# Optimization experiments

Measured on AMD Instinct MI355X. Metric: run time of the kernel, lower is better.

The kernel has to match this reference:

```python
import jax, jax.numpy as jnp
import numpy as np

D_MODEL, D_STATE, D_CONV, EXPAND = 512, 16, 2, 2
D_INNER = EXPAND * D_MODEL          # 1024
DT_RANK = (D_MODEL + 15) // 16      # 32, mamba default ceil(d_model/16)
D_FF = 4 * D_MODEL                  # 2048
B, L = 8, 2048


def _mamba_params(key, prefix):
    ks = jax.random.split(key, 6)
    s = lambda k, shape, sc: (jax.random.normal(k, shape, jnp.float32) * sc)
    return {
        prefix + 'in_proj': s(ks[0], (2 * D_INNER, D_MODEL), 0.02),
        prefix + 'conv_w':  s(ks[1], (D_INNER, 1, D_CONV), 0.2),
        prefix + 'conv_b':  jnp.zeros((D_INNER,), jnp.float32),
        prefix + 'x_proj':  s(ks[2], (DT_RANK + 2 * D_STATE, D_INNER), 0.02),
        prefix + 'dt_w':    s(ks[3], (D_INNER, DT_RANK), 0.05),
        prefix + 'dt_b':    s(ks[4], (D_INNER,), 0.02) - 4.0,  # softplus -> small positive dt
        prefix + 'A_log':   jnp.log(jnp.broadcast_to(jnp.arange(1, D_STATE + 1, dtype=jnp.float32), (D_INNER, D_STATE))),
        prefix + 'Dskip':   jnp.ones((D_INNER,), jnp.float32),
        prefix + 'out_proj': s(ks[5], (D_MODEL, D_INNER), 0.02),
    }


def setup_inputs() -> dict:
    key = jax.random.key(0)
    kx, kf, kb, k1, k2, k3, k4 = jax.random.split(key, 7)
    inp = {'x': jax.random.normal(kx, (B, L, D_MODEL), jnp.float32)}
    inp.update(_mamba_params(kf, 'f_'))
    inp.update(_mamba_params(kb, 'b_'))
    inp.update({
        'ffn_w1': jax.random.normal(k1, (D_FF, D_MODEL), jnp.float32) * 0.02,
        'ffn_b1': jnp.zeros((D_FF,), jnp.float32),
        'ffn_w2': jax.random.normal(k2, (D_MODEL, D_FF), jnp.float32) * 0.02,
        'ffn_b2': jnp.zeros((D_MODEL,), jnp.float32),
        'ln1_g': jnp.ones((D_MODEL,), jnp.float32), 'ln1_b': jnp.zeros((D_MODEL,), jnp.float32),
        'ln2_g': jnp.ones((D_MODEL,), jnp.float32), 'ln2_b': jnp.zeros((D_MODEL,), jnp.float32),
    })
    return inp


def _mamba(x, in_proj, conv_w, conv_b, x_proj, dt_w, dt_b, A_log, Dskip, out_proj):
    """Standard Mamba block (selective SSM). x: (B, L, d_model) -> (B, L, d_model)."""
    Bb = x.shape[0]
    xz = jnp.einsum('bld,ed->ble', x, in_proj)         # (B, L, 2*d_inner)
    xi, z = jnp.split(xz, 2, axis=-1)
    # causal depthwise conv over time
    xc = jnp.transpose(xi, (0, 2, 1))                  # (B, d_inner, L)
    xc = jax.lax.conv_general_dilated(
        xc, conv_w, (1,), [(D_CONV - 1, 0)],
        dimension_numbers=('NCH', 'OIH', 'NCH'), feature_group_count=D_INNER)
    xi = jax.nn.silu(jnp.transpose(xc, (0, 2, 1)) + conv_b)  # (B, L, d_inner)
    # input-dependent dt, B, C
    x_dbl = jnp.einsum('bld,ed->ble', xi, x_proj)
    dt, Bm, Cm = jnp.split(x_dbl, [DT_RANK, DT_RANK + D_STATE], axis=-1)
    dt = jax.nn.softplus(jnp.einsum('blr,dr->bld', dt, dt_w) + dt_b)  # (B, L, d_inner)
    A = -jnp.exp(A_log)                                 # (d_inner, d_state)

    def step(h, inp):
        u_t, dt_t, B_t, C_t = inp                      # (B,d_inner),(B,d_inner),(B,d_state),(B,d_state)
        dA = jnp.exp(dt_t[..., None] * A)              # (B, d_inner, d_state)
        h = dA * h + (dt_t * u_t)[..., None] * B_t[:, None, :]
        y = jnp.einsum('bds,bs->bd', h, C_t)
        return h, y

    h0 = jnp.zeros((Bb, D_INNER, D_STATE), x.dtype)
    xs = (jnp.swapaxes(xi, 0, 1), jnp.swapaxes(dt, 0, 1),
          jnp.swapaxes(Bm, 0, 1), jnp.swapaxes(Cm, 0, 1))
    _, ys = jax.lax.scan(step, h0, xs)                 # ys: (L, B, d_inner)
    y = jnp.swapaxes(ys, 0, 1) + xi * Dskip
    y = y * jax.nn.silu(z)
    return jnp.einsum('bld,ed->ble', y, out_proj)


def _ln(x, g, b):
    m = x.mean(-1, keepdims=True)
    v = ((x - m) ** 2).mean(-1, keepdims=True)
    return (x - m) * jax.lax.rsqrt(v + 1e-5) * g + b


def reference(x,
              f_in_proj, f_conv_w, f_conv_b, f_x_proj, f_dt_w, f_dt_b, f_A_log, f_Dskip, f_out_proj,
              b_in_proj, b_conv_w, b_conv_b, b_x_proj, b_dt_w, b_dt_b, b_A_log, b_Dskip, b_out_proj,
              ffn_w1, ffn_b1, ffn_w2, ffn_b2, ln1_g, ln1_b, ln2_g, ln2_b):
    x_fwd = _mamba(x, f_in_proj, f_conv_w, f_conv_b, f_x_proj, f_dt_w, f_dt_b, f_A_log, f_Dskip, f_out_proj)
    x_bwd = jnp.flip(_mamba(jnp.flip(x, 1), b_in_proj, b_conv_w, b_conv_b, b_x_proj, b_dt_w, b_dt_b, b_A_log, b_Dskip, b_out_proj), 1)
    x = _ln(x + x_fwd + x_bwd, ln1_g, ln1_b)           # dropout = identity (eval)
    h = jax.nn.gelu(jnp.einsum('bld,fd->blf', x, ffn_w1) + ffn_b1, approximate=False)
    x_ffn = jnp.einsum('blf,df->bld', h, ffn_w2) + ffn_b2
    return _ln(x + x_ffn, ln2_g, ln2_b)
```

## Files before the change

### kernel.cpp

```cpp
#include <hip/hip_runtime.h>
#include <hip/hip_bf16.h>

#define BB 8
#define LL 2048
#define DM 512
#define DI 1024
#define DS 16
#define DTR 32
#define DFF 2048
#define BL (BB * LL)
#define CH 64
#define NCH (LL / CH)
#define YL 2048

typedef __hip_bfloat16 bf16;
struct bf4 { bf16 x, y, z, w; };
typedef __attribute__((ext_vector_type(8))) short short8;
typedef __attribute__((ext_vector_type(4))) float floatx4;

__device__ __forceinline__ float silu_f(float x) { return x / (1.f + __expf(-x)); }
__device__ __forceinline__ float softplus_f(float x) { return x > 20.f ? x : log1pf(__expf(x)); }
__device__ __forceinline__ float gelu_f(float x) { return 0.5f * x * (1.f + erff(x * 0.70710678118654752f)); }
__device__ __forceinline__ float b2f(bf16 v) { return __bfloat162float(v); }

__device__ __forceinline__ float4 ld4(const float* p) { return *(const float4*)p; }
__device__ __forceinline__ float4 ld4(const bf16* p) {
    bf4 v = *(const bf4*)p;
    return make_float4(b2f(v.x), b2f(v.y), b2f(v.z), b2f(v.w));
}
__device__ __forceinline__ bf4 pack4(float a, float b, float c, float d) {
    bf4 o; o.x = __float2bfloat16(a); o.y = __float2bfloat16(b);
    o.z = __float2bfloat16(c); o.w = __float2bfloat16(d); return o;
}

__device__ __forceinline__ void gll16(const bf16* g, bf16* l) {
    __builtin_amdgcn_global_load_lds(
        (const __attribute__((address_space(1))) void*)g,
        (__attribute__((address_space(3))) void*)l, 16, 0, 0);
}

enum { EP_BF16, EP_SOFTPLUS, EP_GELU, EP_F32, EP_RESF, EP_BIASRES };

__global__ __launch_bounds__(256) void cvt_kernel(const float* __restrict__ in,
                                                  bf16* __restrict__ out, int n4)
{
    int i = blockIdx.x * 256 + threadIdx.x;
    if (i < n4) {
        float4 v = *(const float4*)(in + (size_t)i * 4);
        *(bf4*)(out + (size_t)i * 4) = pack4(v.x, v.y, v.z, v.w);
    }
}

__global__ __launch_bounds__(256) void cvt_pack_kernel(
    const float* __restrict__ wf, const float* __restrict__ wb,
    bf16* __restrict__ out, int n4)
{
    int i = blockIdx.x * 256 + threadIdx.x;
    if (i < n4) {
        const int pos = i * 4;
        const int n = pos >> 11;
        const int c = pos & 2047;
        const float* src = (c < 1024) ? (wf + (size_t)n * 1024 + c)
                                      : (wb + (size_t)n * 1024 + (c - 1024));
        float4 v = *(const float4*)src;
        *(bf4*)(out + (size_t)pos) = pack4(v.x, v.y, v.z, v.w);
    }
}

template <int EPI, int BN>
__global__ __launch_bounds__(256) void gemm_mfma(
    const bf16* __restrict__ A, int lda,
    const bf16* __restrict__ W, int ldb,
    void* __restrict__ Cv, int ldc, int K,
    const float* __restrict__ bias, const void* __restrict__ resv)
{
    constexpr int BM = 128, BK = 32;
    constexpr int NT = BN / 32;
    constexpr int ACH_W = 2;
    constexpr int WCH_W = (BN / 16) / 4;
    constexpr int PITCH = BN + 8;
    constexpr int TILE_B = BM * 64 + BN * 64;
    constexpr int STG_B = 32 * PITCH * 4;
    constexpr int SMEM_B = TILE_B > STG_B ? TILE_B : STG_B;
    __shared__ __align__(1024) char smem[SMEM_B];
    bf16* sA = (bf16*)smem;
    bf16* sW = (bf16*)(smem + BM * 64);

    const int tid = threadIdx.x;
    const int wv = tid >> 6, ln = tid & 63;
    const int rloc = ln >> 2;
    const int kperm = (ln & 3) ^ ((ln >> 3) & 3);
    const int c = ln & 15, q4 = ln >> 4;
    const int swz8 = 8 * (q4 ^ ((c >> 1) & 3));
    const int m0 = blockIdx.x * BM, n0 = blockIdx.y * BN;
    const int wm = (wv >> 1) * 64, wn = (wv & 1) * (BN / 2);

    floatx4 acc[4][NT] = {};

    for (int k0 = 0; k0 < K; k0 += BK) {
        __syncthreads();
#pragma unroll
        for (int q = 0; q < ACH_W; ++q) {
            const int chunk = wv * ACH_W + q;
            gll16(A + (size_t)(m0 + chunk * 16 + rloc) * lda + k0 + kperm * 8,
                  sA + chunk * 512);
        }
#pragma unroll
        for (int q = 0; q < WCH_W; ++q) {
            const int chunk = wv * WCH_W + q;
            gll16(W + (size_t)(n0 + chunk * 16 + rloc) * ldb + k0 + kperm * 8,
                  sW + chunk * 512);
        }
        __syncthreads();

        short8 af[4], wf[NT];
#pragma unroll
        for (int i = 0; i < 4; ++i)
            af[i] = *(const short8*)(sA + (wm + i * 16 + c) * 32 + swz8);
#pragma unroll
        for (int j = 0; j < NT; ++j)
            wf[j] = *(const short8*)(sW + (wn + j * 16 + c) * 32 + swz8);
#pragma unroll
        for (int i = 0; i < 4; ++i)
#pragma unroll
            for (int j = 0; j < NT; ++j)
                acc[i][j] = __builtin_amdgcn_mfma_f32_16x16x32_bf16(
                    af[i], wf[j], acc[i][j], 0, 0, 0);
    }

    constexpr int ELEMS = (32 * BN) / 256;
    constexpr int TPR = BN / ELEMS;
    float* sC = (float*)smem;
    const int row_l = tid / TPR;
    const int cg = (tid % TPR) * ELEMS;
    const int mg = m0 + (row_l & 15) + ((row_l >> 4) * 64);

#pragma unroll
    for (int i = 0; i < 4; ++i) {
        __syncthreads();
#pragma unroll
        for (int j = 0; j < NT; ++j)
#pragma unroll
            for (int r = 0; r < 4; ++r)
                sC[((wv >> 1) * 16 + q4 * 4 + r) * PITCH + wn + j * 16 + c] = acc[i][j][r];
        __syncthreads();

        const int m = mg + i * 16;
        const int nb = n0 + cg;
        const size_t co = (size_t)m * ldc + nb;
        float v[ELEMS];
#pragma unroll
        for (int e = 0; e < ELEMS; ++e) v[e] = sC[row_l * PITCH + cg + e];

        if constexpr (EPI == EP_BF16 || EPI == EP_GELU) {
            bf16 ov[ELEMS];
#pragma unroll
            for (int e = 0; e < ELEMS; ++e) {
                float t = v[e];
                if constexpr (EPI == EP_GELU) t = gelu_f(t + bias[nb + e]);
                ov[e] = __float2bfloat16(t);
            }
#pragma unroll
            for (int q = 0; q < ELEMS / 8; ++q)
                *(uint4*)((bf16*)Cv + co + q * 8) = *(const uint4*)(ov + q * 8);
        } else {
#pragma unroll
            for (int e = 0; e < ELEMS; ++e) {
                if constexpr (EPI == EP_RESF)
                    v[e] += ((const float*)resv)[co + e];
                else if constexpr (EPI == EP_BIASRES)
                    v[e] += bias[nb + e] + b2f(((const bf16*)resv)[co + e]);
            }
#pragma unroll
            for (int q = 0; q < ELEMS / 4; ++q) {
                float4 o = {v[q * 4 + 0], v[q * 4 + 1], v[q * 4 + 2], v[q * 4 + 3]};
                *(float4*)((float*)Cv + co + q * 4) = o;
            }
        }
    }
}

template <int EPI, typename TA>
__global__ __launch_bounds__(256) void gemm_nt(
    const TA* __restrict__ A, int lda,
    const float* __restrict__ W, int ldb,
    void* __restrict__ Cv, int ldc,
    int K,
    const float* __restrict__ bias,
    const void* __restrict__ resv)
{
    __shared__ float As[16][64];
    __shared__ float Bs[16][64];
    const int tid = threadIdx.x;
    const int tx = tid & 15, ty = tid >> 4;
    const int m0 = blockIdx.y * 64, n0 = blockIdx.x * 64;
    const int lrow = tid >> 2;
    const int lcol = (tid & 3) << 2;

    const TA* Ap = A + (size_t)(m0 + lrow) * lda + lcol;
    const float* Bp = W + (size_t)(n0 + lrow) * ldb + lcol;

    float acc[4][4] = {};

    for (int k0 = 0; k0 < K; k0 += 16) {
        float4 av = ld4(Ap + k0);
        float4 bv = ld4(Bp + k0);
        __syncthreads();
        As[lcol + 0][lrow] = av.x; As[lcol + 1][lrow] = av.y;
        As[lcol + 2][lrow] = av.z; As[lcol + 3][lrow] = av.w;
        Bs[lcol + 0][lrow] = bv.x; Bs[lcol + 1][lrow] = bv.y;
        Bs[lcol + 2][lrow] = bv.z; Bs[lcol + 3][lrow] = bv.w;
        __syncthreads();
#pragma unroll
        for (int kk = 0; kk < 16; ++kk) {
            float4 a4 = *(const float4*)(&As[kk][ty << 2]);
            float4 b4 = *(const float4*)(&Bs[kk][tx << 2]);
            float aa[4] = {a4.x, a4.y, a4.z, a4.w};
            float bb[4] = {b4.x, b4.y, b4.z, b4.w};
#pragma unroll
            for (int i = 0; i < 4; ++i)
#pragma unroll
                for (int j = 0; j < 4; ++j)
                    acc[i][j] = fmaf(aa[i], bb[j], acc[i][j]);
        }
    }

#pragma unroll
    for (int i = 0; i < 4; ++i) {
        const int m = m0 + (ty << 2) + i;
        const int n = n0 + (tx << 2);
        float v[4] = {acc[i][0], acc[i][1], acc[i][2], acc[i][3]};
        const size_t co = (size_t)m * ldc + n;
        if constexpr (EPI == EP_SOFTPLUS) {
            *(bf4*)((bf16*)Cv + co) = pack4(
                softplus_f(v[0] + bias[n + 0]), softplus_f(v[1] + bias[n + 1]),
                softplus_f(v[2] + bias[n + 2]), softplus_f(v[3] + bias[n + 3]));
        } else if constexpr (EPI == EP_F32) {
            float4 o = {v[0], v[1], v[2], v[3]};
            *(float4*)((float*)Cv + co) = o;
        }
    }
}

__global__ __launch_bounds__(256) void conv_silu_kernel(
    const bf16* __restrict__ xz, const float* __restrict__ cw,
    const float* __restrict__ cb, bf16* __restrict__ xic, int nbr)
{
    const int idx = blockIdx.x * 256 + threadIdx.x;
    const int c4 = (idx & 255) << 2;
    const int row = idx >> 8;
    const int l = row & (LL - 1);
    const int lnbr = l + nbr;
    const bool valid = (lnbr >= 0) && (lnbr < LL);

    const bf16* pc = xz + (size_t)row * (2 * DI) + c4;
    float4 cur = ld4(pc);
    float4 prv = make_float4(0.f, 0.f, 0.f, 0.f);
    if (valid) prv = ld4(pc + (ptrdiff_t)nbr * (2 * DI));

    float w0[4], w1[4];
#pragma unroll
    for (int q = 0; q < 4; ++q) { w0[q] = cw[(c4 + q) * 2]; w1[q] = cw[(c4 + q) * 2 + 1]; }
    float4 bb = ld4(cb + c4);

    *(bf4*)(xic + (size_t)row * DI + c4) = pack4(
        silu_f(fmaf(w0[0], prv.x, fmaf(w1[0], cur.x, bb.x))),
        silu_f(fmaf(w0[1], prv.y, fmaf(w1[1], cur.y, bb.y))),
        silu_f(fmaf(w0[2], prv.z, fmaf(w1[2], cur.z, bb.z))),
        silu_f(fmaf(w0[3], prv.w, fmaf(w1[3], cur.w, bb.w))));
}

__global__ __launch_bounds__(256) void scan_p1(
    const bf16* __restrict__ xic, const bf16* __restrict__ ydt,
    const float* __restrict__ xdb, const float* __restrict__ A_log,
    float* __restrict__ SD, float* __restrict__ H, int t0, int tstep)
{
    const int g = blockIdx.x * 256 + threadIdx.x;
    const int d = g & (DI - 1);
    const int rest = g >> 10;
    const int chunk = rest & (NCH - 1);
    const int b = rest >> 5;

    float a[DS], h[DS];
    bool fast = true;
#pragma unroll
    for (int s = 0; s < DS; ++s) {
        a[s] = -__expf(A_log[d * DS + s]);
        h[s] = 0.f;
        fast = fast && (fabsf(a[s] + (float)(s + 1)) < 1e-3f * (s + 1));
    }

    __shared__ float sB[CH][DS];
    for (int i = threadIdx.x; i < CH * DS; i += 256) {
        const int it = i >> 4, s = i & 15;
        const int t = t0 + (chunk * CH + it) * tstep;
        sB[it][s] = xdb[((size_t)(b * LL + t)) * 64 + DTR + s];
    }
    __syncthreads();

    float sumdt = 0.f;
    if (fast) {
        for (int it = 0; it < CH; ++it) {
            const int t = t0 + (chunk * CH + it) * tstep;
            const size_t row = (size_t)(b * LL + t);
            const float dtv = b2f(ydt[row * YL + d]);
            const float u = b2f(xic[row * DI + d]);
            sumdt += dtv;
            const float du = dtv * u;
            const float e = __expf(-dtv);
            float dA = 1.f;
#pragma unroll
            for (int s = 0; s < DS; ++s) {
                dA *= e;
                h[s] = fmaf(dA, h[s], du * sB[it][s]);
            }
        }
    } else {
        for (int it = 0; it < CH; ++it) {
            const int t = t0 + (chunk * CH + it) * tstep;
            const size_t row = (size_t)(b * LL + t);
            const float dtv = b2f(ydt[row * YL + d]);
            const float u = b2f(xic[row * DI + d]);
            sumdt += dtv;
            const float du = dtv * u;
#pragma unroll
            for (int s = 0; s < DS; ++s)
                h[s] = fmaf(__expf(dtv * a[s]), h[s], du * sB[it][s]);
        }
    }
    SD[((size_t)(b * NCH + chunk)) * DI + d] = sumdt;
    const size_t base = ((size_t)((b * NCH + chunk) * DS)) * DI + d;
#pragma unroll
    for (int s = 0; s < DS; ++s)
        H[base + (size_t)s * DI] = h[s];
}

__global__ __launch_bounds__(256) void scan_p2(
    const float* __restrict__ SD, float* __restrict__ H,
    const float* __restrict__ A_log)
{
    const int g = blockIdx.x * 256 + threadIdx.x;
    const int d = g & (DI - 1);
    const int rest = g >> 10;
    const int s = rest & 15;
    const int b = rest >> 4;
    const float a = -__expf(A_log[d * DS + s]);
    float h = 0.f;
    for (int c = 0; c < NCH; ++c) {
        const float sd = SD[((size_t)(b * NCH + c)) * DI + d];
        const size_t idx = ((size_t)((b * NCH + c) * DS + s)) * DI + d;
        const float Pv = __expf(a * sd);
        const float Hv = H[idx];
        H[idx] = h;
        h = fmaf(Pv, h, Hv);
    }
}

__global__ __launch_bounds__(256) void scan_p3(
    const bf16* __restrict__ xic, const bf16* __restrict__ xz,
    const float* __restrict__ xdb, bf16* __restrict__ dty,
    const float* __restrict__ A_log, const float* __restrict__ Dskip,
    const float* __restrict__ H, int t0, int tstep)
{
    const int g = blockIdx.x * 256 + threadIdx.x;
    const int d = g & (DI - 1);
    const int rest = g >> 10;
    const int chunk = rest & (NCH - 1);
    const int b = rest >> 5;

    float a[DS], h[DS];
    bool fast = true;
    const size_t base = ((size_t)((b * NCH + chunk) * DS)) * DI + d;
#pragma unroll
    for (int s = 0; s < DS; ++s) {
        a[s] = -__expf(A_log[d * DS + s]);
        h[s] = H[base + (size_t)s * DI];
        fast = fast && (fabsf(a[s] + (float)(s + 1)) < 1e-3f * (s + 1));
    }
    const float dsk = Dskip[d];

    __shared__ float sBC[CH][2 * DS];
    for (int i = threadIdx.x; i < CH * 2 * DS; i += 256) {
        const int it = i >> 5, j = i & 31;
        const int t = t0 + (chunk * CH + it) * tstep;
        sBC[it][j] = xdb[((size_t)(b * LL + t)) * 64 + DTR + j];
    }
    __syncthreads();

    if (fast) {
        for (int it = 0; it < CH; ++it) {
            const int t = t0 + (chunk * CH + it) * tstep;
            const size_t row = (size_t)(b * LL + t);
            const float dtv = b2f(dty[row * YL + d]);
            const float u = b2f(xic[row * DI + d]);
            const float zv = b2f(xz[row * (2 * DI) + DI + d]);
            const float du = dtv * u;
            const float e = __expf(-dtv);
            float dA = 1.f, y = 0.f;
#pragma unroll
            for (int s = 0; s < DS; ++s) {
                dA *= e;
                h[s] = fmaf(dA, h[s], du * sBC[it][s]);
                y = fmaf(h[s], sBC[it][DS + s], y);
            }
            y = fmaf(u, dsk, y);
            dty[row * YL + d] = __float2bfloat16(y * silu_f(zv));
        }
    } else {
        for (int it = 0; it < CH; ++it) {
            const int t = t0 + (chunk * CH + it) * tstep;
            const size_t row = (size_t)(b * LL + t);
            const float dtv = b2f(dty[row * YL + d]);
            const float u = b2f(xic[row * DI + d]);
            const float zv = b2f(xz[row * (2 * DI) + DI + d]);
            const float du = dtv * u;
            float y = 0.f;
#pragma unroll
            for (int s = 0; s < DS; ++s) {
                h[s] = fmaf(__expf(dtv * a[s]), h[s], du * sBC[it][s]);
                y = fmaf(h[s], sBC[it][DS + s], y);
            }
            y = fmaf(u, dsk, y);
            dty[row * YL + d] = __float2bfloat16(y * silu_f(zv));
        }
    }
}

template <int OUTF>
__global__ __launch_bounds__(256) void ln_kernel(
    const float* __restrict__ in, const float* __restrict__ g,
    const float* __restrict__ bta, void* __restrict__ outv)
{
    const int row = blockIdx.x;
    const int t = threadIdx.x;
    const float* p = in + (size_t)row * DM;
    const float v0 = p[t];
    const float v1 = p[t + 256];
    float sm = v0 + v1;
    float sq = v0 * v0 + v1 * v1;
#pragma unroll
    for (int off = 32; off > 0; off >>= 1) {
        sm += __shfl_xor(sm, off);
        sq += __shfl_xor(sq, off);
    }
    __shared__ float red[8];
    const int w = t >> 6;
    if ((t & 63) == 0) { red[w] = sm; red[4 + w] = sq; }
    __syncthreads();
    sm = red[0] + red[1] + red[2] + red[3];
    sq = red[4] + red[5] + red[6] + red[7];
    const float mean = sm * (1.f / DM);
    const float var = sq * (1.f / DM) - mean * mean;
    const float rstd = rsqrtf(var + 1e-5f);
    const float o0 = (v0 - mean) * rstd * g[t] + bta[t];
    const float o1 = (v1 - mean) * rstd * g[t + 256] + bta[t + 256];
    if constexpr (OUTF == 0) {
        bf16* out = (bf16*)outv;
        out[(size_t)row * DM + t] = __float2bfloat16(o0);
        out[(size_t)row * DM + t + 256] = __float2bfloat16(o1);
    } else {
        float* out = (float*)outv;
        out[(size_t)row * DM + t] = o0;
        out[(size_t)row * DM + t + 256] = o1;
    }
}

extern "C" void kernel_launch(void* const* d_in, const int* in_sizes, int n_in,
                              void* d_out, int out_size, void* d_ws, size_t ws_size,
                              hipStream_t stream)
{
    const float* x = (const float*)d_in[0];
    const float* ffn_w1 = (const float*)d_in[19];
    const float* ffn_b1 = (const float*)d_in[20];
    const float* ffn_w2 = (const float*)d_in[21];
    const float* ffn_b2 = (const float*)d_in[22];
    const float* ln1_g = (const float*)d_in[23];
    const float* ln1_b = (const float*)d_in[24];
    const float* ln2_g = (const float*)d_in[25];
    const float* ln2_b = (const float*)d_in[26];

    char* p = (char*)d_ws;
    auto alloc = [&](size_t bytes) { void* r = (void*)p; p += (bytes + 255) & ~(size_t)255; return r; };
    bf16* xz    = (bf16*)alloc((size_t)BL * 2048 * 2);
    bf16* xic   = (bf16*)alloc((size_t)BL * DI * 2);
    bf16* ybuf  = (bf16*)alloc((size_t)BL * YL * 2);
    float* xdb  = (float*)alloc((size_t)BL * 64 * 4);
    float* sum  = (float*)alloc((size_t)BL * DM * 4);
    bf16* x1    = (bf16*)alloc((size_t)BL * DM * 2);
    bf16* xb    = (bf16*)alloc((size_t)BL * DM * 2);
    float* SD   = (float*)alloc((size_t)BB * NCH * DI * 4);
    float* Hc   = (float*)alloc((size_t)BB * NCH * DS * DI * 4);
    bf16* wip[2], *wxp[2];
    for (int d = 0; d < 2; ++d) {
        wip[d] = (bf16*)alloc((size_t)2 * DI * DM * 2);
        wxp[d] = (bf16*)alloc((size_t)64 * DI * 2);
    }
    bf16* wopcat = (bf16*)alloc((size_t)DM * YL * 2);
    bf16* w1b = (bf16*)alloc((size_t)DFF * DM * 2);
    bf16* w2b = (bf16*)alloc((size_t)DM * DFF * 2);

    auto cvt = [&](const float* src, bf16* dst, size_t n) {
        int n4 = (int)(n / 4);
        cvt_kernel<<<(n4 + 255) / 256, 256, 0, stream>>>(src, dst, n4);
    };
    cvt(x, xb, (size_t)BL * DM);
    for (int d = 0; d < 2; ++d) {
        const int o = 1 + d * 9;
        cvt((const float*)d_in[o + 0], wip[d], (size_t)2 * DI * DM);
        cvt((const float*)d_in[o + 3], wxp[d], (size_t)64 * DI);
    }
    cvt_pack_kernel<<<(DM * YL / 4 + 255) / 256, 256, 0, stream>>>(
        (const float*)d_in[9], (const float*)d_in[18], wopcat, DM * YL / 4);
    cvt(ffn_w1, w1b, (size_t)DFF * DM);
    cvt(ffn_w2, w2b, (size_t)DM * DFF);

    const dim3 blk(256);
    for (int dir = 0; dir < 2; ++dir) {
        const int o = 1 + dir * 9;
        const float* conv_w = (const float*)d_in[o + 1];
        const float* conv_b = (const float*)d_in[o + 2];
        const float* dt_w   = (const float*)d_in[o + 4];
        const float* dt_b   = (const float*)d_in[o + 5];
        const float* A_log  = (const float*)d_in[o + 6];
        const float* Dskip  = (const float*)d_in[o + 7];

        const int nbr = (dir == 0) ? -1 : +1;
        const int t0 = (dir == 0) ? 0 : (LL - 1);
        const int tstep = (dir == 0) ? 1 : -1;
        bf16* ydt = ybuf + (size_t)dir * 1024;

        gemm_mfma<EP_BF16, 128><<<dim3(BL / 128, (2 * DI) / 128), blk, 0, stream>>>(
            xb, DM, wip[dir], DM, xz, 2 * DI, DM, nullptr, nullptr);
        conv_silu_kernel<<<BL, blk, 0, stream>>>(xz, conv_w, conv_b, xic, nbr);
        gemm_mfma<EP_F32, 64><<<dim3(BL / 128, 1), blk, 0, stream>>>(
            xic, DI, wxp[dir], DI, xdb, 64, DI, nullptr, nullptr);
        gemm_nt<EP_SOFTPLUS, float><<<dim3(DI / 64, BL / 64), blk, 0, stream>>>(
            xdb, 64, dt_w, DTR, ydt, YL, DTR, dt_b, nullptr);

        scan_p1<<<(BB * NCH * DI) / 256, blk, 0, stream>>>(
            xic, ydt, xdb, A_log, SD, Hc, t0, tstep);
        scan_p2<<<(BB * DS * DI) / 256, blk, 0, stream>>>(SD, Hc, A_log);
        scan_p3<<<(BB * NCH * DI) / 256, blk, 0, stream>>>(
            xic, xz, xdb, ydt, A_log, Dskip, Hc, t0, tstep);
    }

    gemm_mfma<EP_RESF, 128><<<dim3(BL / 128, DM / 128), blk, 0, stream>>>(
        ybuf, YL, wopcat, YL, sum, DM, YL, nullptr, x);

    ln_kernel<0><<<BL, blk, 0, stream>>>(sum, ln1_g, ln1_b, x1);
    gemm_mfma<EP_GELU, 128><<<dim3(BL / 128, DFF / 128), blk, 0, stream>>>(
        x1, DM, w1b, DM, xz, DFF, DM, ffn_b1, nullptr);
    gemm_mfma<EP_BIASRES, 128><<<dim3(BL / 128, DM / 128), blk, 0, stream>>>(
        xz, DFF, w2b, DFF, sum, DM, DFF, ffn_b2, x1);
    ln_kernel<1><<<BL, blk, 0, stream>>>(sum, ln2_g, ln2_b, d_out);
}
```

Before: 885.3 us.

## Move dt projection to MFMA GEMM with bf16 xdb and halve scan chunk

Replaces the fp32 SIMT gemm_nt for the dt projection with the MFMA GEMM, adding a softplus epilogue and converting dt_w to bf16. The x_proj output (dt, B, C) is now stored as bf16 instead of fp32, and the scan kernels read it with conversion. The scan chunk length is halved so the scan has more parallel chunks, and the chunk-state buffer now aliases the sum buffer, which is free at that point. This trades some precision in dt, B and C and a larger scan_p2 pass for faster projection and more scan parallelism.

```diff
diff --git a/kernel.cpp b/kernel.cpp
--- a/kernel.cpp
+++ b/kernel.cpp
@@ -9,7 +9,7 @@
 #define DTR 32
 #define DFF 2048
 #define BL (BB * LL)
-#define CH 64
+#define CH 32
 #define NCH (LL / CH)
 #define YL 2048
 
@@ -152,12 +152,13 @@
 #pragma unroll
         for (int e = 0; e < ELEMS; ++e) v[e] = sC[row_l * PITCH + cg + e];
 
-        if constexpr (EPI == EP_BF16 || EPI == EP_GELU) {
+        if constexpr (EPI == EP_BF16 || EPI == EP_GELU || EPI == EP_SOFTPLUS) {
             bf16 ov[ELEMS];
 #pragma unroll
             for (int e = 0; e < ELEMS; ++e) {
                 float t = v[e];
                 if constexpr (EPI == EP_GELU) t = gelu_f(t + bias[nb + e]);
+                if constexpr (EPI == EP_SOFTPLUS) t = softplus_f(t + bias[nb + e]);
                 ov[e] = __float2bfloat16(t);
             }
 #pragma unroll
@@ -176,68 +177,6 @@
                 float4 o = {v[q * 4 + 0], v[q * 4 + 1], v[q * 4 + 2], v[q * 4 + 3]};
                 *(float4*)((float*)Cv + co + q * 4) = o;
             }
-        }
-    }
-}
-
-template <int EPI, typename TA>
-__global__ __launch_bounds__(256) void gemm_nt(
-    const TA* __restrict__ A, int lda,
-    const float* __restrict__ W, int ldb,
-    void* __restrict__ Cv, int ldc,
-    int K,
-    const float* __restrict__ bias,
-    const void* __restrict__ resv)
-{
-    __shared__ float As[16][64];
-    __shared__ float Bs[16][64];
-    const int tid = threadIdx.x;
-    const int tx = tid & 15, ty = tid >> 4;
-    const int m0 = blockIdx.y * 64, n0 = blockIdx.x * 64;
-    const int lrow = tid >> 2;
-    const int lcol = (tid & 3) << 2;
-
-    const TA* Ap = A + (size_t)(m0 + lrow) * lda + lcol;
-    const float* Bp = W + (size_t)(n0 + lrow) * ldb + lcol;
-
-    float acc[4][4] = {};
-
-    for (int k0 = 0; k0 < K; k0 += 16) {
-        float4 av = ld4(Ap + k0);
-        float4 bv = ld4(Bp + k0);
-        __syncthreads();
-        As[lcol + 0][lrow] = av.x; As[lcol + 1][lrow] = av.y;
-        As[lcol + 2][lrow] = av.z; As[lcol + 3][lrow] = av.w;
-        Bs[lcol + 0][lrow] = bv.x; Bs[lcol + 1][lrow] = bv.y;
-        Bs[lcol + 2][lrow] = bv.z; Bs[lcol + 3][lrow] = bv.w;
-        __syncthreads();
-#pragma unroll
-        for (int kk = 0; kk < 16; ++kk) {
-            float4 a4 = *(const float4*)(&As[kk][ty << 2]);
-            float4 b4 = *(const float4*)(&Bs[kk][tx << 2]);
-            float aa[4] = {a4.x, a4.y, a4.z, a4.w};
-            float bb[4] = {b4.x, b4.y, b4.z, b4.w};
-#pragma unroll
-            for (int i = 0; i < 4; ++i)
-#pragma unroll
-                for (int j = 0; j < 4; ++j)
-                    acc[i][j] = fmaf(aa[i], bb[j], acc[i][j]);
-        }
-    }
-
-#pragma unroll
-    for (int i = 0; i < 4; ++i) {
-        const int m = m0 + (ty << 2) + i;
-        const int n = n0 + (tx << 2);
-        float v[4] = {acc[i][0], acc[i][1], acc[i][2], acc[i][3]};
-        const size_t co = (size_t)m * ldc + n;
-        if constexpr (EPI == EP_SOFTPLUS) {
-            *(bf4*)((bf16*)Cv + co) = pack4(
-                softplus_f(v[0] + bias[n + 0]), softplus_f(v[1] + bias[n + 1]),
-                softplus_f(v[2] + bias[n + 2]), softplus_f(v[3] + bias[n + 3]));
-        } else if constexpr (EPI == EP_F32) {
-            float4 o = {v[0], v[1], v[2], v[3]};
-            *(float4*)((float*)Cv + co) = o;
         }
     }
 }
@@ -272,14 +211,14 @@
 
 __global__ __launch_bounds__(256) void scan_p1(
     const bf16* __restrict__ xic, const bf16* __restrict__ ydt,
-    const float* __restrict__ xdb, const float* __restrict__ A_log,
+    const bf16* __restrict__ xdb, const float* __restrict__ A_log,
     float* __restrict__ SD, float* __restrict__ H, int t0, int tstep)
 {
     const int g = blockIdx.x * 256 + threadIdx.x;
     const int d = g & (DI - 1);
     const int rest = g >> 10;
     const int chunk = rest & (NCH - 1);
-    const int b = rest >> 5;
+    const int b = rest >> 6;
 
     float a[DS], h[DS];
     bool fast = true;
@@ -294,7 +233,7 @@
     for (int i = threadIdx.x; i < CH * DS; i += 256) {
         const int it = i >> 4, s = i & 15;
         const int t = t0 + (chunk * CH + it) * tstep;
-        sB[it][s] = xdb[((size_t)(b * LL + t)) * 64 + DTR + s];
+        sB[it][s] = b2f(xdb[((size_t)(b * LL + t)) * 64 + DTR + s]);
     }
     __syncthreads();
 
@@ -358,7 +297,7 @@
 
 __global__ __launch_bounds__(256) void scan_p3(
     const bf16* __restrict__ xic, const bf16* __restrict__ xz,
-    const float* __restrict__ xdb, bf16* __restrict__ dty,
+    const bf16* __restrict__ xdb, bf16* __restrict__ dty,
     const float* __restrict__ A_log, const float* __restrict__ Dskip,
     const float* __restrict__ H, int t0, int tstep)
 {
@@ -366,7 +305,7 @@
     const int d = g & (DI - 1);
     const int rest = g >> 10;
     const int chunk = rest & (NCH - 1);
-    const int b = rest >> 5;
+    const int b = rest >> 6;
 
     float a[DS], h[DS];
     bool fast = true;
@@ -383,7 +322,7 @@
     for (int i = threadIdx.x; i < CH * 2 * DS; i += 256) {
         const int it = i >> 5, j = i & 31;
         const int t = t0 + (chunk * CH + it) * tstep;
-        sBC[it][j] = xdb[((size_t)(b * LL + t)) * 64 + DTR + j];
+        sBC[it][j] = b2f(xdb[((size_t)(b * LL + t)) * 64 + DTR + j]);
     }
     __syncthreads();
 
@@ -484,16 +423,17 @@
     bf16* xz    = (bf16*)alloc((size_t)BL * 2048 * 2);
     bf16* xic   = (bf16*)alloc((size_t)BL * DI * 2);
     bf16* ybuf  = (bf16*)alloc((size_t)BL * YL * 2);
-    float* xdb  = (float*)alloc((size_t)BL * 64 * 4);
+    bf16* xdbb  = (bf16*)alloc((size_t)BL * 64 * 2);
     float* sum  = (float*)alloc((size_t)BL * DM * 4);
+    float* Hc   = sum;
     bf16* x1    = (bf16*)alloc((size_t)BL * DM * 2);
     bf16* xb    = (bf16*)alloc((size_t)BL * DM * 2);
     float* SD   = (float*)alloc((size_t)BB * NCH * DI * 4);
-    float* Hc   = (float*)alloc((size_t)BB * NCH * DS * DI * 4);
-    bf16* wip[2], *wxp[2];
+    bf16* wip[2], *wxp[2], *wdt[2];
     for (int d = 0; d < 2; ++d) {
         wip[d] = (bf16*)alloc((size_t)2 * DI * DM * 2);
         wxp[d] = (bf16*)alloc((size_t)64 * DI * 2);
+        wdt[d] = (bf16*)alloc((size_t)DI * DTR * 2);
     }
     bf16* wopcat = (bf16*)alloc((size_t)DM * YL * 2);
     bf16* w1b = (bf16*)alloc((size_t)DFF * DM * 2);
@@ -508,6 +448,7 @@
         const int o = 1 + d * 9;
         cvt((const float*)d_in[o + 0], wip[d], (size_t)2 * DI * DM);
         cvt((const float*)d_in[o + 3], wxp[d], (size_t)64 * DI);
+        cvt((const float*)d_in[o + 4], wdt[d], (size_t)DI * DTR);
     }
     cvt_pack_kernel<<<(DM * YL / 4 + 255) / 256, 256, 0, stream>>>(
         (const float*)d_in[9], (const float*)d_in[18], wopcat, DM * YL / 4);
@@ -519,7 +460,6 @@
         const int o = 1 + dir * 9;
         const float* conv_w = (const float*)d_in[o + 1];
         const float* conv_b = (const float*)d_in[o + 2];
-        const float* dt_w   = (const float*)d_in[o + 4];
         const float* dt_b   = (const float*)d_in[o + 5];
         const float* A_log  = (const float*)d_in[o + 6];
         const float* Dskip  = (const float*)d_in[o + 7];
@@ -532,16 +472,16 @@
         gemm_mfma<EP_BF16, 128><<<dim3(BL / 128, (2 * DI) / 128), blk, 0, stream>>>(
             xb, DM, wip[dir], DM, xz, 2 * DI, DM, nullptr, nullptr);
         conv_silu_kernel<<<BL, blk, 0, stream>>>(xz, conv_w, conv_b, xic, nbr);
-        gemm_mfma<EP_F32, 64><<<dim3(BL / 128, 1), blk, 0, stream>>>(
-            xic, DI, wxp[dir], DI, xdb, 64, DI, nullptr, nullptr);
-        gemm_nt<EP_SOFTPLUS, float><<<dim3(DI / 64, BL / 64), blk, 0, stream>>>(
-            xdb, 64, dt_w, DTR, ydt, YL, DTR, dt_b, nullptr);
+        gemm_mfma<EP_BF16, 64><<<dim3(BL / 128, 1), blk, 0, stream>>>(
+            xic, DI, wxp[dir], DI, xdbb, 64, DI, nullptr, nullptr);
+        gemm_mfma<EP_SOFTPLUS, 128><<<dim3(BL / 128, DI / 128), blk, 0, stream>>>(
+            xdbb, 64, wdt[dir], DTR, ydt, YL, DTR, dt_b, nullptr);
 
         scan_p1<<<(BB * NCH * DI) / 256, blk, 0, stream>>>(
-            xic, ydt, xdb, A_log, SD, Hc, t0, tstep);
+            xic, ydt, xdbb, A_log, SD, Hc, t0, tstep);
         scan_p2<<<(BB * DS * DI) / 256, blk, 0, stream>>>(SD, Hc, A_log);
         scan_p3<<<(BB * NCH * DI) / 256, blk, 0, stream>>>(
-            xic, xz, xdb, ydt, A_log, Dskip, Hc, t0, tstep);
+            xic, xz, xdbb, ydt, A_log, Dskip, Hc, t0, tstep);
     }
 
     gemm_mfma<EP_RESF, 128><<<dim3(BL / 128, DM / 128), blk, 0, stream>>>(
```

Result: no change. 889.8 us (+0.5%).
